# Kernel tuning notes

Measured on AMD Instinct MI355X. Metric: run time of the kernel, lower is better.

## Reference

```python
import jax, jax.numpy as jnp
import numpy as np

B, S, D = 2, 2048, 1024
H = 16
HD = D // H  # 64
SCALE = HD ** -0.5


def setup_inputs() -> dict:
    key = jax.random.key(0)
    k1, k2, k3 = jax.random.split(key, 3)
    x = jax.random.normal(k1, (B, S, D), dtype=jnp.float32)
    w_qkv = jax.random.normal(k2, (D, 3 * D), dtype=jnp.float32) * (D ** -0.5)
    w_out = jax.random.normal(k3, (D, D), dtype=jnp.float32) * (D ** -0.5)
    return {"x": x, "w_qkv": w_qkv, "w_out": w_out}


def reference(x, w_qkv, w_out):
    batch, seq, hidden = x.shape
    qkv = jnp.einsum('bsd,de->bse', x, w_qkv)  # (B,S,3D)
    q, k, v = jnp.split(qkv, 3, axis=-1)
    # (B,H,S,HD)
    q = q.reshape(batch, seq, H, HD).transpose(0, 2, 1, 3)
    k = k.reshape(batch, seq, H, HD).transpose(0, 2, 1, 3)
    v = v.reshape(batch, seq, H, HD).transpose(0, 2, 1, 3)
    # full (B,H,S,S) scores, as in the original module
    scores = jnp.einsum('bhqd,bhkd->bhqk', q, k) * SCALE
    causal = jnp.tril(jnp.ones((seq, seq), dtype=bool))
    scores = jnp.where(causal[None, None], scores, -jnp.inf)
    attn = jax.nn.softmax(scores, axis=-1)
    out = jnp.einsum('bhqk,bhkd->bhqd', attn, v)
    out = out.transpose(0, 2, 1, 3).reshape(batch, seq, hidden)
    return jnp.einsum('bsd,de->bse', out, w_out)
```

## Files before the change

kernel.cpp:

```cpp
#include <hip/hip_runtime.h>
#include <hip/hip_bf16.h>
#include <stdint.h>

typedef unsigned short u16;
typedef unsigned int u32;
typedef __attribute__((ext_vector_type(8))) short short8;
typedef __attribute__((ext_vector_type(4))) short short4e;
typedef __attribute__((ext_vector_type(4))) float f32x4;
typedef __attribute__((ext_vector_type(16))) float f32x16;

constexpr int CB = 2, CS = 2048, CD = 1024, CH = 16, CHD = 64;
constexpr float CSCALE = 0.125f;
constexpr float SC2 = 0.125f * 1.44269504088896f;
constexpr float DEFER_THR = 11.0f;

__device__ __forceinline__ u16 f2bf(float f) {
    unsigned u = __float_as_uint(f);
    u += 0x7fffu + ((u >> 16) & 1u);
    return (u16)(u >> 16);
}

#if __has_builtin(__builtin_amdgcn_exp2f)
#define EXP2F(x) __builtin_amdgcn_exp2f(x)
#else
#define EXP2F(x) exp2f(x)
#endif

__device__ __forceinline__ u32 pkbf(float a, float b) {
    u32 r;
    asm("v_cvt_pk_bf16_f32 %0, %1, %2" : "=v"(r) : "v"(a), "v"(b));
    return r;
}

__global__ __launch_bounds__(256) void cvt_x(const float* __restrict__ X, u16* __restrict__ Y) {
    const int i = (blockIdx.x * 256 + threadIdx.x) * 8;
    const float4 v0 = *(const float4*)(X + i);
    const float4 v1 = *(const float4*)(X + i + 4);
    short8 r;
    r[0] = (short)f2bf(v0.x); r[1] = (short)f2bf(v0.y);
    r[2] = (short)f2bf(v0.z); r[3] = (short)f2bf(v0.w);
    r[4] = (short)f2bf(v1.x); r[5] = (short)f2bf(v1.y);
    r[6] = (short)f2bf(v1.z); r[7] = (short)f2bf(v1.w);
    *(short8*)(Y + i) = r;
}

__global__ __launch_bounds__(256) void txw(const float* __restrict__ W, u16* __restrict__ Bt,
                                           int ldw) {
    __shared__ u16 T[64][80];
    const int t = threadIdx.x;
    const int n0 = blockIdx.x * 64, k0 = blockIdx.y * 64;
    const int r = t >> 4, c4 = (t & 15) * 4;
#pragma unroll
    for (int p = 0; p < 4; ++p) {
        const int kr = r + p * 16;
        const float4 v = *(const float4*)(W + (size_t)(k0 + kr) * ldw + n0 + c4);
        T[c4 + 0][kr] = f2bf(v.x); T[c4 + 1][kr] = f2bf(v.y);
        T[c4 + 2][kr] = f2bf(v.z); T[c4 + 3][kr] = f2bf(v.w);
    }
    __syncthreads();
    const int rr = t >> 2, cc = (t & 3) * 16;
    const short8 a = *(const short8*)((const char*)&T[0][0] + rr * 160 + cc * 2);
    const short8 b = *(const short8*)((const char*)&T[0][0] + rr * 160 + cc * 2 + 16);
    u16* dst = Bt + (size_t)(n0 + rr) * 1024 + k0 + cc;
    *(short8*)dst = a;
    *(short8*)(dst + 8) = b;
}

__global__ __launch_bounds__(256) void gemm_mfma(
    const u16* __restrict__ A, const u16* __restrict__ Bt, int mode,
    u16* __restrict__ Qws, u16* __restrict__ Kws, u16* __restrict__ Vtws,
    float* __restrict__ Cf)
{
    __shared__ u16 SB[2][8192];
    const int tid = threadIdx.x;
    const int w = tid >> 6, lane = tid & 63;
    const int l15 = lane & 15, l4 = lane >> 4;
    const int wr = w >> 1, wc = w & 1;
    const int n0 = blockIdx.x * 128, m0 = blockIdx.y * 128;

    f32x4 acc[4][4];
    const f32x4 zf = {0.f, 0.f, 0.f, 0.f};
#pragma unroll
    for (int i = 0; i < 4; ++i)
#pragma unroll
        for (int j = 0; j < 4; ++j) acc[i][j] = zf;

    short8 stg[4];
#define GEMM_ISSUE(K0)                                                          \
    {                                                                           \
        _Pragma("unroll")                                                       \
        for (int it = 0; it < 4; ++it) {                                        \
            const int c = tid + it * 256;                                       \
            const u16* src;                                                     \
            if (c < 512) { const int row = c >> 2, cs = c & 3;                  \
                src = A + (size_t)(m0 + row) * 1024 + (K0) + cs * 8; }          \
            else { const int c2 = c - 512; const int row = c2 >> 2, cs = c2 & 3;\
                src = Bt + (size_t)(n0 + row) * 1024 + (K0) + cs * 8; }         \
            stg[it] = *(const short8*)src;                                      \
        }                                                                       \
    }
#define GEMM_WRITE(BUF)                                                         \
    {                                                                           \
        _Pragma("unroll")                                                       \
        for (int it = 0; it < 4; ++it) {                                        \
            const int c = tid + it * 256;                                       \
            *(short8*)&SB[BUF][c * 8] = stg[it];                                \
        }                                                                       \
    }

    GEMM_ISSUE(0);
    GEMM_WRITE(0);
    __syncthreads();

    for (int t = 0; t < 32; ++t) {
        const int cur = t & 1;
        if (t < 31) GEMM_ISSUE((t + 1) * 32);

        const u16* Al = &SB[cur][0];
        const u16* Bl = &SB[cur][4096];
        short8 a[4], b[4];
#pragma unroll
        for (int i = 0; i < 4; ++i)
            a[i] = *(const short8*)(Al + (wr * 64 + i * 16 + l15) * 32 + l4 * 8);
#pragma unroll
        for (int j = 0; j < 4; ++j)
            b[j] = *(const short8*)(Bl + (wc * 64 + j * 16 + l15) * 32 + l4 * 8);
#pragma unroll
        for (int i = 0; i < 4; ++i)
#pragma unroll
            for (int j = 0; j < 4; ++j)
                acc[i][j] = __builtin_amdgcn_mfma_f32_16x16x32_bf16(a[i], b[j], acc[i][j], 0, 0, 0);

        if (t < 31) GEMM_WRITE(cur ^ 1);
        __syncthreads();
    }

    if (mode == 1) {
#pragma unroll
        for (int i = 0; i < 4; ++i)
#pragma unroll
            for (int j = 0; j < 4; ++j)
#pragma unroll
                for (int r = 0; r < 4; ++r)
                    Cf[(size_t)(m0 + wr * 64 + i * 16 + l4 * 4 + r) * 1024 +
                       n0 + wc * 64 + j * 16 + l15] = acc[i][j][r];
    } else {
        const int e0 = n0 + wc * 64;
        const int which = e0 >> 10;
        const int h = (e0 >> 6) & 15;
        const int b = m0 >> 11;
        const int sbase = (m0 & 2047) + wr * 64;
        if (which == 2) {
#pragma unroll
            for (int i = 0; i < 4; ++i)
#pragma unroll
                for (int j = 0; j < 4; ++j) {
                    const int hd = j * 16 + l15;
                    const int s4 = sbase + i * 16 + l4 * 4;
                    short4e p;
                    p[0] = (short)f2bf(acc[i][j][0]); p[1] = (short)f2bf(acc[i][j][1]);
                    p[2] = (short)f2bf(acc[i][j][2]); p[3] = (short)f2bf(acc[i][j][3]);
                    *(short4e*)(Vtws + ((size_t)(b * 16 + h) * 64 + hd) * 2048 + s4) = p;
                }
        } else {
            u16* dst = which ? Kws : Qws;
#pragma unroll
            for (int i = 0; i < 4; ++i)
#pragma unroll
                for (int j = 0; j < 4; ++j)
#pragma unroll
                    for (int r = 0; r < 4; ++r) {
                        const int s = sbase + i * 16 + l4 * 4 + r;
                        dst[((size_t)(b * 16 + h) * 2048 + s) * 64 + j * 16 + l15] =
                            f2bf(acc[i][j][r]);
                    }
        }
    }
#undef GEMM_ISSUE
#undef GEMM_WRITE
}

__global__ __launch_bounds__(256) void attn_mfma32(
    const u16* __restrict__ Qg, const u16* __restrict__ Kg,
    const u16* __restrict__ Vtg, u16* __restrict__ Og)
{
    __shared__ u16 KV[2][8192];
    __shared__ float Aw[4][32];

    const int tid = threadIdx.x;
    const int w = tid >> 6, lane = tid & 63;
    const int l31 = lane & 31, hi = lane >> 5;
    const int bid = blockIdx.x;
    const int kq = bid >> 5, bh = bid & 31;
    const int qt = (kq < 8) ? (15 - kq) : (kq - 8);

    const u16* Qp = Qg + (size_t)bh * CS * CHD;
    const u16* Kp = Kg + (size_t)bh * CS * CHD;
    const u16* Vp = Vtg + (size_t)bh * CHD * CS;
    const int q0w = qt * 128 + w * 32;
    const int qrow = q0w + l31;

    short8 qf[4];
#pragma unroll
    for (int c = 0; c < 4; ++c)
        qf[c] = *(const short8*)(Qp + (size_t)qrow * 64 + c * 16 + hi * 8);

    f32x16 o0, o1;
#pragma unroll
    for (int r = 0; r < 16; ++r) { o0[r] = 0.f; o1[r] = 0.f; }
    float m_run = -1e30f, l_run = 0.f;

    const int nkt = 2 * qt + 2;
    short8 stg[4];

#define ATTN_ISSUE(K0)                                                           \
    {                                                                            \
        _Pragma("unroll")                                                        \
        for (int it = 0; it < 4; ++it) {                                         \
            const int c = tid + it * 256;                                        \
            const int ob = c * 16;                                               \
            const u16* src;                                                      \
            if (ob < 8192) { const int row = ob >> 7, cs = (ob >> 4) & 7;        \
                src = Kp + (size_t)((K0) + row) * 64 + cs * 8; }                 \
            else { const int o2 = ob - 8192; const int row = o2 >> 7,            \
                cs = (o2 >> 4) & 7;                                              \
                src = Vp + (size_t)row * CS + (K0) + cs * 8; }                   \
            stg[it] = *(const short8*)src;                                       \
        }                                                                        \
    }
#define ATTN_WRITE(BUF)                                                          \
    {                                                                            \
        _Pragma("unroll")                                                        \
        for (int it = 0; it < 4; ++it) {                                         \
            const int c = tid + it * 256;                                        \
            const int ob = c * 16;                                               \
            int db;                                                              \
            if (ob < 8192) { const int row = ob >> 7; db = ob ^ ((row & 7) << 4); } \
            else { const int o2 = ob - 8192; const int row = o2 >> 7;            \
                db = 8192 + (o2 ^ ((row & 7) << 4)); }                           \
            *(short8*)((char*)&KV[BUF][0] + db) = stg[it];                       \
        }                                                                        \
    }

    ATTN_ISSUE(0);
    ATTN_WRITE(0);
    __syncthreads();

    for (int kt = 0; kt < nkt; ++kt) {
        const int k0 = kt * 64;
        const int cur = kt & 1;
        if (kt + 1 < nkt) ATTN_ISSUE((kt + 1) * 64);

        if (k0 <= q0w + 31) {
            const char* Kl = (const char*)&KV[cur][0];
            const char* Vl = (const char*)&KV[cur][4096];

            f32x16 s0, s1;
#pragma unroll
            for (int r = 0; r < 16; ++r) { s0[r] = 0.f; s1[r] = 0.f; }
#pragma unroll
            for (int c = 0; c < 4; ++c) {
                const int row = l31;
                const short8 kf = *(const short8*)(Kl + row * 128 +
                                    ((c * 32 + hi * 16) ^ ((row & 7) << 4)));
                s0 = __builtin_amdgcn_mfma_f32_32x32x16_bf16(kf, qf[c], s0, 0, 0, 0);
            }
#pragma unroll
            for (int c = 0; c < 4; ++c) {
                const int row = 32 + l31;
                const short8 kf = *(const short8*)(Kl + row * 128 +
                                    ((c * 32 + hi * 16) ^ ((row & 7) << 4)));
                s1 = __builtin_amdgcn_mfma_f32_32x32x16_bf16(kf, qf[c], s1, 0, 0, 0);
            }

            const bool edge = (k0 + 63 > q0w);
            float pmax = -1e30f;
#pragma unroll
            for (int r = 0; r < 16; ++r) {
                float a0 = s0[r] * SC2, a1 = s1[r] * SC2;
                if (edge) {
                    const int koff = (r & 3) + 8 * (r >> 2) + 4 * hi;
                    if (k0 + koff > qrow) a0 = -1e30f;
                    if (k0 + 32 + koff > qrow) a1 = -1e30f;
                }
                s0[r] = a0; s1[r] = a1;
                pmax = fmaxf(pmax, fmaxf(a0, a1));
            }
            pmax = fmaxf(pmax, __shfl_xor(pmax, 32));

            if (!__all(pmax - m_run <= DEFER_THR)) {
                const float mn = fmaxf(m_run, pmax);
                const float al = EXP2F(m_run - mn);
                l_run *= al;
                m_run = mn;
                if (lane < 32) Aw[w][l31] = al;
                asm volatile("" ::: "memory");
#pragma unroll
                for (int g = 0; g < 4; ++g) {
                    const f32x4 av = *(const f32x4*)&Aw[w][g * 8 + hi * 4];
#pragma unroll
                    for (int c = 0; c < 4; ++c) {
                        o0[g * 4 + c] *= av[c];
                        o1[g * 4 + c] *= av[c];
                    }
                }
            }

            float lsum = 0.f;
#pragma unroll
            for (int r = 0; r < 16; ++r) {
                const float p0 = EXP2F(s0[r] - m_run);
                const float p1 = EXP2F(s1[r] - m_run);
                s0[r] = p0; s1[r] = p1;
                lsum += p0 + p1;
            }
            lsum += __shfl_xor(lsum, 32);
            l_run += lsum;

#pragma unroll
            for (int ks = 0; ks < 4; ++ks) {
                const int rb = (ks & 1) * 8;
                const f32x16& sv = (ks < 2) ? s0 : s1;
                u32 w0 = pkbf(sv[rb + 0], sv[rb + 1]);
                u32 w1 = pkbf(sv[rb + 2], sv[rb + 3]);
                u32 w2 = pkbf(sv[rb + 4], sv[rb + 5]);
                u32 w3 = pkbf(sv[rb + 6], sv[rb + 7]);
                asm("v_permlane32_swap_b32 %0, %1" : "+v"(w0), "+v"(w2));
                asm("v_permlane32_swap_b32 %0, %1" : "+v"(w1), "+v"(w3));
                union { u32 uw[4]; short8 v; } pu;
                pu.uw[0] = w0; pu.uw[1] = w1; pu.uw[2] = w2; pu.uw[3] = w3;
                const short8 pa = pu.v;

                const int vr0 = l31, vr1 = 32 + l31;
                const short8 v0 = *(const short8*)(Vl + vr0 * 128 +
                                    ((ks * 32 + hi * 16) ^ ((vr0 & 7) << 4)));
                const short8 v1 = *(const short8*)(Vl + vr1 * 128 +
                                    ((ks * 32 + hi * 16) ^ ((vr1 & 7) << 4)));
                o0 = __builtin_amdgcn_mfma_f32_32x32x16_bf16(pa, v0, o0, 0, 0, 0);
                o1 = __builtin_amdgcn_mfma_f32_32x32x16_bf16(pa, v1, o1, 0, 0, 0);
            }
        }

        if (kt + 1 < nkt) ATTN_WRITE(cur ^ 1);
        __syncthreads();
    }

    if (lane < 32) Aw[w][l31] = 1.f / l_run;
    asm volatile("" ::: "memory");
    const int b = bh >> 4, h = bh & 15;
#pragma unroll
    for (int g = 0; g < 4; ++g) {
        const f32x4 iv = *(const f32x4*)&Aw[w][g * 8 + hi * 4];
#pragma unroll
        for (int c = 0; c < 4; ++c) {
            const int q = q0w + 8 * g + 4 * hi + c;
            u16* dst = Og + ((size_t)(b * CS + q)) * CD + h * 64 + l31;
            dst[0]  = f2bf(o0[g * 4 + c] * iv[c]);
            dst[32] = f2bf(o1[g * 4 + c] * iv[c]);
        }
    }
#undef ATTN_ISSUE
#undef ATTN_WRITE
}

extern "C" void kernel_launch(void* const* d_in, const int* in_sizes, int n_in,
                              void* d_out, int out_size, void* d_ws, size_t ws_size,
                              hipStream_t stream)
{
    const float* x     = (const float*)d_in[0];
    const float* w_qkv = (const float*)d_in[1];
    const float* w_out = (const float*)d_in[2];
    float* out = (float*)d_out;

    u16* xb    = (u16*)d_ws;
    u16* wqkvT = xb    + (size_t)4096 * 1024;
    u16* woutT = wqkvT + (size_t)3072 * 1024;
    u16* Qws   = woutT + (size_t)1024 * 1024;
    u16* Kws   = Qws   + (size_t)32 * 2048 * 64;
    u16* Vtws  = Kws   + (size_t)32 * 2048 * 64;
    u16* Ob    = Vtws  + (size_t)32 * 2048 * 64;

    cvt_x<<<2048, 256, 0, stream>>>(x, xb);
    txw<<<dim3(48, 16), 256, 0, stream>>>(w_qkv, wqkvT, 3072);
    txw<<<dim3(16, 16), 256, 0, stream>>>(w_out, woutT, 1024);

    gemm_mfma<<<dim3(24, 32), 256, 0, stream>>>(xb, wqkvT, 0, Qws, Kws, Vtws, nullptr);
    attn_mfma32<<<512, 256, 0, stream>>>(Qws, Kws, Vtws, Ob);
    gemm_mfma<<<dim3(8, 32), 256, 0, stream>>>(Ob, woutT, 1, nullptr, nullptr, nullptr, out);
}
```

Baseline: 202.8 us.

## Use direct global-to-LDS loads in GEMM and LDS-free single-wave attention

The GEMM now stages tiles with global_load_lds straight into shared memory instead of going through registers, and raises wave priority around the MFMA block. The attention kernel is rewritten as one wave per 32-query chunk that reads K and V directly from global memory, with no LDS and no block barriers. It skips the upper 32-key half of diagonal tiles and folds the softmax scale into Q at the projection epilogue. Without LDS staging, K and V are re-read from global/L2 by every wave, so this trades shared-memory reuse for more parallelism and no synchronisation.

```diff
diff --git a/kernel.cpp b/kernel.cpp
--- a/kernel.cpp
+++ b/kernel.cpp
@@ -10,7 +10,6 @@
 typedef __attribute__((ext_vector_type(16))) float f32x16;
 
 constexpr int CB = 2, CS = 2048, CD = 1024, CH = 16, CHD = 64;
-constexpr float CSCALE = 0.125f;
 constexpr float SC2 = 0.125f * 1.44269504088896f;
 constexpr float DEFER_THR = 11.0f;
 
@@ -85,8 +84,7 @@
 #pragma unroll
         for (int j = 0; j < 4; ++j) acc[i][j] = zf;
 
-    short8 stg[4];
-#define GEMM_ISSUE(K0)                                                          \
+#define GEMM_STAGE(BUF, K0)                                                     \
     {                                                                           \
         _Pragma("unroll")                                                       \
         for (int it = 0; it < 4; ++it) {                                        \
@@ -96,25 +94,19 @@
                 src = A + (size_t)(m0 + row) * 1024 + (K0) + cs * 8; }          \
             else { const int c2 = c - 512; const int row = c2 >> 2, cs = c2 & 3;\
                 src = Bt + (size_t)(n0 + row) * 1024 + (K0) + cs * 8; }         \
-            stg[it] = *(const short8*)src;                                      \
+            __builtin_amdgcn_global_load_lds(                                   \
+                (const __attribute__((address_space(1))) unsigned int*)src,     \
+                (__attribute__((address_space(3))) unsigned int*)&SB[BUF][c*8], \
+                16, 0, 0);                                                      \
         }                                                                       \
     }
-#define GEMM_WRITE(BUF)                                                         \
-    {                                                                           \
-        _Pragma("unroll")                                                       \
-        for (int it = 0; it < 4; ++it) {                                        \
-            const int c = tid + it * 256;                                       \
-            *(short8*)&SB[BUF][c * 8] = stg[it];                                \
-        }                                                                       \
-    }
-
-    GEMM_ISSUE(0);
-    GEMM_WRITE(0);
+
+    GEMM_STAGE(0, 0);
     __syncthreads();
 
     for (int t = 0; t < 32; ++t) {
         const int cur = t & 1;
-        if (t < 31) GEMM_ISSUE((t + 1) * 32);
+        if (t < 31) GEMM_STAGE(cur ^ 1, (t + 1) * 32);
 
         const u16* Al = &SB[cur][0];
         const u16* Bl = &SB[cur][4096];
@@ -125,13 +117,13 @@
 #pragma unroll
         for (int j = 0; j < 4; ++j)
             b[j] = *(const short8*)(Bl + (wc * 64 + j * 16 + l15) * 32 + l4 * 8);
+        __builtin_amdgcn_s_setprio(1);
 #pragma unroll
         for (int i = 0; i < 4; ++i)
 #pragma unroll
             for (int j = 0; j < 4; ++j)
                 acc[i][j] = __builtin_amdgcn_mfma_f32_16x16x32_bf16(a[i], b[j], acc[i][j], 0, 0, 0);
-
-        if (t < 31) GEMM_WRITE(cur ^ 1);
+        __builtin_amdgcn_s_setprio(0);
         __syncthreads();
     }
 
@@ -164,6 +156,7 @@
                 }
         } else {
             u16* dst = which ? Kws : Qws;
+            const float qsc = which ? 1.0f : SC2;
 #pragma unroll
             for (int i = 0; i < 4; ++i)
 #pragma unroll
@@ -172,33 +165,28 @@
                     for (int r = 0; r < 4; ++r) {
                         const int s = sbase + i * 16 + l4 * 4 + r;
                         dst[((size_t)(b * 16 + h) * 2048 + s) * 64 + j * 16 + l15] =
-                            f2bf(acc[i][j][r]);
+                            f2bf(acc[i][j][r] * qsc);
                     }
         }
     }
-#undef GEMM_ISSUE
-#undef GEMM_WRITE
-}
-
-__global__ __launch_bounds__(256) void attn_mfma32(
+#undef GEMM_STAGE
+}
+
+__global__ __launch_bounds__(64, 4) void attn_nolds(
     const u16* __restrict__ Qg, const u16* __restrict__ Kg,
     const u16* __restrict__ Vtg, u16* __restrict__ Og)
 {
-    __shared__ u16 KV[2][8192];
-    __shared__ float Aw[4][32];
-
-    const int tid = threadIdx.x;
-    const int w = tid >> 6, lane = tid & 63;
+    const int lane = threadIdx.x;
     const int l31 = lane & 31, hi = lane >> 5;
     const int bid = blockIdx.x;
-    const int kq = bid >> 5, bh = bid & 31;
-    const int qt = (kq < 8) ? (15 - kq) : (kq - 8);
+    const int bh = bid & 31;
+    const int qchunk = 63 - (bid >> 5);
+    const int q0 = qchunk * 32;
+    const int qrow = q0 + l31;
 
     const u16* Qp = Qg + (size_t)bh * CS * CHD;
     const u16* Kp = Kg + (size_t)bh * CS * CHD;
     const u16* Vp = Vtg + (size_t)bh * CHD * CS;
-    const int q0w = qt * 128 + w * 32;
-    const int qrow = q0w + l31;
 
     short8 qf[4];
 #pragma unroll
@@ -210,157 +198,130 @@
     for (int r = 0; r < 16; ++r) { o0[r] = 0.f; o1[r] = 0.f; }
     float m_run = -1e30f, l_run = 0.f;
 
-    const int nkt = 2 * qt + 2;
-    short8 stg[4];
-
-#define ATTN_ISSUE(K0)                                                           \
-    {                                                                            \
-        _Pragma("unroll")                                                        \
-        for (int it = 0; it < 4; ++it) {                                         \
-            const int c = tid + it * 256;                                        \
-            const int ob = c * 16;                                               \
-            const u16* src;                                                      \
-            if (ob < 8192) { const int row = ob >> 7, cs = (ob >> 4) & 7;        \
-                src = Kp + (size_t)((K0) + row) * 64 + cs * 8; }                 \
-            else { const int o2 = ob - 8192; const int row = o2 >> 7,            \
-                cs = (o2 >> 4) & 7;                                              \
-                src = Vp + (size_t)row * CS + (K0) + cs * 8; }                   \
-            stg[it] = *(const short8*)src;                                       \
-        }                                                                        \
-    }
-#define ATTN_WRITE(BUF)                                                          \
-    {                                                                            \
-        _Pragma("unroll")                                                        \
-        for (int it = 0; it < 4; ++it) {                                         \
-            const int c = tid + it * 256;                                        \
-            const int ob = c * 16;                                               \
-            int db;                                                              \
-            if (ob < 8192) { const int row = ob >> 7; db = ob ^ ((row & 7) << 4); } \
-            else { const int o2 = ob - 8192; const int row = o2 >> 7;            \
-                db = 8192 + (o2 ^ ((row & 7) << 4)); }                           \
-            *(short8*)((char*)&KV[BUF][0] + db) = stg[it];                       \
-        }                                                                        \
-    }
-
-    ATTN_ISSUE(0);
-    ATTN_WRITE(0);
-    __syncthreads();
+    const int nkt = (qchunk >> 1) + 1;
 
     for (int kt = 0; kt < nkt; ++kt) {
         const int k0 = kt * 64;
-        const int cur = kt & 1;
-        if (kt + 1 < nkt) ATTN_ISSUE((kt + 1) * 64);
-
-        if (k0 <= q0w + 31) {
-            const char* Kl = (const char*)&KV[cur][0];
-            const char* Vl = (const char*)&KV[cur][4096];
-
-            f32x16 s0, s1;
-#pragma unroll
-            for (int r = 0; r < 16; ++r) { s0[r] = 0.f; s1[r] = 0.f; }
+        const bool edge = (k0 + 63 > q0);
+        const bool do_hi = (k0 + 32 <= q0 + 31);
+
+        const u16* Kb = Kp + (size_t)(k0 + l31) * 64 + hi * 8;
+        f32x16 s0, s1;
+#pragma unroll
+        for (int r = 0; r < 16; ++r) s0[r] = 0.f;
+        __builtin_amdgcn_s_setprio(1);
+#pragma unroll
+        for (int c = 0; c < 4; ++c) {
+            const short8 kf = *(const short8*)(Kb + c * 16);
+            s0 = __builtin_amdgcn_mfma_f32_32x32x16_bf16(kf, qf[c], s0, 0, 0, 0);
+        }
+        if (do_hi) {
+#pragma unroll
+            for (int r = 0; r < 16; ++r) s1[r] = 0.f;
 #pragma unroll
             for (int c = 0; c < 4; ++c) {
-                const int row = l31;
-                const short8 kf = *(const short8*)(Kl + row * 128 +
-                                    ((c * 32 + hi * 16) ^ ((row & 7) << 4)));
-                s0 = __builtin_amdgcn_mfma_f32_32x32x16_bf16(kf, qf[c], s0, 0, 0, 0);
-            }
-#pragma unroll
-            for (int c = 0; c < 4; ++c) {
-                const int row = 32 + l31;
-                const short8 kf = *(const short8*)(Kl + row * 128 +
-                                    ((c * 32 + hi * 16) ^ ((row & 7) << 4)));
+                const short8 kf = *(const short8*)(Kb + 32 * 64 + c * 16);
                 s1 = __builtin_amdgcn_mfma_f32_32x32x16_bf16(kf, qf[c], s1, 0, 0, 0);
             }
-
-            const bool edge = (k0 + 63 > q0w);
-            float pmax = -1e30f;
+        }
+        __builtin_amdgcn_s_setprio(0);
+
+        float pmax = -1e30f;
+#pragma unroll
+        for (int r = 0; r < 16; ++r) {
+            float a0 = s0[r];
+            if (edge) {
+                const int koff = (r & 3) + 8 * (r >> 2) + 4 * hi;
+                if (k0 + koff > qrow) a0 = -1e30f;
+            }
+            s0[r] = a0;
+            pmax = fmaxf(pmax, a0);
+        }
+        if (do_hi) {
 #pragma unroll
             for (int r = 0; r < 16; ++r) {
-                float a0 = s0[r] * SC2, a1 = s1[r] * SC2;
+                float a1 = s1[r];
                 if (edge) {
                     const int koff = (r & 3) + 8 * (r >> 2) + 4 * hi;
-                    if (k0 + koff > qrow) a0 = -1e30f;
                     if (k0 + 32 + koff > qrow) a1 = -1e30f;
                 }
-                s0[r] = a0; s1[r] = a1;
-                pmax = fmaxf(pmax, fmaxf(a0, a1));
-            }
-            pmax = fmaxf(pmax, __shfl_xor(pmax, 32));
-
-            if (!__all(pmax - m_run <= DEFER_THR)) {
-                const float mn = fmaxf(m_run, pmax);
-                const float al = EXP2F(m_run - mn);
-                l_run *= al;
-                m_run = mn;
-                if (lane < 32) Aw[w][l31] = al;
-                asm volatile("" ::: "memory");
-#pragma unroll
-                for (int g = 0; g < 4; ++g) {
-                    const f32x4 av = *(const f32x4*)&Aw[w][g * 8 + hi * 4];
-#pragma unroll
-                    for (int c = 0; c < 4; ++c) {
-                        o0[g * 4 + c] *= av[c];
-                        o1[g * 4 + c] *= av[c];
-                    }
-                }
-            }
-
-            float lsum = 0.f;
+                s1[r] = a1;
+                pmax = fmaxf(pmax, a1);
+            }
+        }
+        pmax = fmaxf(pmax, __shfl_xor(pmax, 32));
+
+        if (!__all(pmax - m_run <= DEFER_THR)) {
+            const float mn = fmaxf(m_run, pmax);
+            const float al = EXP2F(m_run - mn);
+            l_run *= al;
+            m_run = mn;
 #pragma unroll
             for (int r = 0; r < 16; ++r) {
-                const float p0 = EXP2F(s0[r] - m_run);
+                const int qq = (r & 3) + 8 * (r >> 2) + 4 * hi;
+                const float av = __shfl(al, qq);
+                o0[r] *= av; o1[r] *= av;
+            }
+        }
+
+        float lsum = 0.f;
+#pragma unroll
+        for (int r = 0; r < 16; ++r) {
+            const float p0 = EXP2F(s0[r] - m_run);
+            s0[r] = p0; lsum += p0;
+        }
+        if (do_hi) {
+#pragma unroll
+            for (int r = 0; r < 16; ++r) {
                 const float p1 = EXP2F(s1[r] - m_run);
-                s0[r] = p0; s1[r] = p1;
-                lsum += p0 + p1;
-            }
-            lsum += __shfl_xor(lsum, 32);
-            l_run += lsum;
-
-#pragma unroll
-            for (int ks = 0; ks < 4; ++ks) {
-                const int rb = (ks & 1) * 8;
-                const f32x16& sv = (ks < 2) ? s0 : s1;
-                u32 w0 = pkbf(sv[rb + 0], sv[rb + 1]);
-                u32 w1 = pkbf(sv[rb + 2], sv[rb + 3]);
-                u32 w2 = pkbf(sv[rb + 4], sv[rb + 5]);
-                u32 w3 = pkbf(sv[rb + 6], sv[rb + 7]);
-                asm("v_permlane32_swap_b32 %0, %1" : "+v"(w0), "+v"(w2));
-                asm("v_permlane32_swap_b32 %0, %1" : "+v"(w1), "+v"(w3));
-                union { u32 uw[4]; short8 v; } pu;
-                pu.uw[0] = w0; pu.uw[1] = w1; pu.uw[2] = w2; pu.uw[3] = w3;
-                const short8 pa = pu.v;
-
-                const int vr0 = l31, vr1 = 32 + l31;
-                const short8 v0 = *(const short8*)(Vl + vr0 * 128 +
-                                    ((ks * 32 + hi * 16) ^ ((vr0 & 7) << 4)));
-                const short8 v1 = *(const short8*)(Vl + vr1 * 128 +
-                                    ((ks * 32 + hi * 16) ^ ((vr1 & 7) << 4)));
-                o0 = __builtin_amdgcn_mfma_f32_32x32x16_bf16(pa, v0, o0, 0, 0, 0);
-                o1 = __builtin_amdgcn_mfma_f32_32x32x16_bf16(pa, v1, o1, 0, 0, 0);
-            }
-        }
-
-        if (kt + 1 < nkt) ATTN_WRITE(cur ^ 1);
-        __syncthreads();
-    }
-
-    if (lane < 32) Aw[w][l31] = 1.f / l_run;
-    asm volatile("" ::: "memory");
+                s1[r] = p1; lsum += p1;
+            }
+        }
+        lsum += __shfl_xor(lsum, 32);
+        l_run += lsum;
+
+        const u16* Vb  = Vp + (size_t)l31 * CS + k0 + hi * 8;
+        const u16* Vb2 = Vb + (size_t)32 * CS;
+#define PV_STEP(KS, SV)                                                          \
+        {                                                                        \
+            const int rb = ((KS) & 1) * 8;                                       \
+            u32 w0 = pkbf(SV[rb + 0], SV[rb + 1]);                               \
+            u32 w1 = pkbf(SV[rb + 2], SV[rb + 3]);                               \
+            u32 w2 = pkbf(SV[rb + 4], SV[rb + 5]);                               \
+            u32 w3 = pkbf(SV[rb + 6], SV[rb + 7]);                               \
+            asm("v_permlane32_swap_b32 %0, %1" : "+v"(w0), "+v"(w2));            \
+            asm("v_permlane32_swap_b32 %0, %1" : "+v"(w1), "+v"(w3));            \
+            union { u32 uw[4]; short8 v; } pu;                                   \
+            pu.uw[0] = w0; pu.uw[1] = w1; pu.uw[2] = w2; pu.uw[3] = w3;          \
+            const short8 pa = pu.v;                                              \
+            const short8 v0 = *(const short8*)(Vb  + (KS) * 16);                 \
+            const short8 v1 = *(const short8*)(Vb2 + (KS) * 16);                 \
+            __builtin_amdgcn_s_setprio(1);                                       \
+            o0 = __builtin_amdgcn_mfma_f32_32x32x16_bf16(pa, v0, o0, 0, 0, 0);   \
+            o1 = __builtin_amdgcn_mfma_f32_32x32x16_bf16(pa, v1, o1, 0, 0, 0);   \
+            __builtin_amdgcn_s_setprio(0);                                       \
+        }
+        PV_STEP(0, s0)
+        PV_STEP(1, s0)
+        if (do_hi) {
+            PV_STEP(2, s1)
+            PV_STEP(3, s1)
+        }
+#undef PV_STEP
+    }
+
+    const float invl = 1.f / l_run;
     const int b = bh >> 4, h = bh & 15;
 #pragma unroll
-    for (int g = 0; g < 4; ++g) {
-        const f32x4 iv = *(const f32x4*)&Aw[w][g * 8 + hi * 4];
+    for (int g = 0; g < 4; ++g)
 #pragma unroll
         for (int c = 0; c < 4; ++c) {
-            const int q = q0w + 8 * g + 4 * hi + c;
-            u16* dst = Og + ((size_t)(b * CS + q)) * CD + h * 64 + l31;
-            dst[0]  = f2bf(o0[g * 4 + c] * iv[c]);
-            dst[32] = f2bf(o1[g * 4 + c] * iv[c]);
-        }
-    }
-#undef ATTN_ISSUE
-#undef ATTN_WRITE
+            const int qq = 8 * g + 4 * hi + c;
+            const float av = __shfl(invl, qq);
+            u16* dst = Og + ((size_t)(b * CS + q0 + qq)) * CD + h * 64 + l31;
+            dst[0]  = f2bf(o0[g * 4 + c] * av);
+            dst[32] = f2bf(o1[g * 4 + c] * av);
+        }
 }
 
 extern "C" void kernel_launch(void* const* d_in, const int* in_sizes, int n_in,
@@ -385,6 +346,6 @@
     txw<<<dim3(16, 16), 256, 0, stream>>>(w_out, woutT, 1024);
 
     gemm_mfma<<<dim3(24, 32), 256, 0, stream>>>(xb, wqkvT, 0, Qws, Kws, Vtws, nullptr);
-    attn_mfma32<<<512, 256, 0, stream>>>(Qws, Kws, Vtws, Ob);
+    attn_nolds<<<2048, 64, 0, stream>>>(Qws, Kws, Vtws, Ob);
     gemm_mfma<<<dim3(8, 32), 256, 0, stream>>>(Ob, woutT, 1, nullptr, nullptr, nullptr, out);
 }
```

Measured after the change: 233.0 us. +14.9%, slower.
